# Performance work log

Measured on AMD Instinct MI355X. Metric: run time of the kernel, lower is better.

The kernel has to match this reference:

```python
import jax, jax.numpy as jnp
import numpy as np

BZ, DC, NR = 65536, 512, 1024
MARGIN = 1.0
MASK_VAL = 1000.0

def _l2_normalize(x, eps=1e-12):
    # F.normalize: x / max(||x||_2, eps) along last dim
    n = jnp.sqrt(jnp.sum(x * x, axis=-1, keepdims=True))
    return x / jnp.maximum(n, eps)

def setup_inputs() -> dict:
    key = jax.random.key(0)
    k1, k2, k3 = jax.random.split(key, 3)
    wo = jax.random.normal(k1, (BZ, DC), dtype=jnp.float32)
    rel_weight = jax.random.normal(k2, (NR, DC), dtype=jnp.float32)
    in_y = jax.random.randint(k3, (BZ,), 0, NR, dtype=jnp.int64)
    return {"wo": wo, "rel_weight": rel_weight, "in_y": in_y}

def reference(wo, rel_weight, in_y):
    wo_n = _l2_normalize(wo)                       # [bz, dc]
    rw_n = _l2_normalize(rel_weight)               # [nr, dc]
    # ||a-b|| for unit vectors: sqrt(2 - 2 a.b); avoids [bz,nr,dc] intermediate
    sim = jnp.einsum('bd,nd->bn', wo_n, rw_n)      # [bz, nr]
    all_distance = jnp.sqrt(jnp.maximum(2.0 - 2.0 * sim, 0.0))
    b = jnp.arange(wo.shape[0])
    masked = all_distance.at[b, in_y].add(MASK_VAL)  # mask out the true class
    neg_idx = jnp.argmin(masked, axis=1)           # nearest wrong relation
    # gather instead of one-hot matmul; dist to gathered row equals row of all_distance
    pos_distance = all_distance[b, in_y]
    neg_distance = all_distance[b, neg_idx]
    loss = jnp.mean(pos_distance + jnp.clip(MARGIN - neg_distance, 0.0, 9999.0))
    return loss
```

## Files before the change

### kernel.cpp

```cpp
#include <hip/hip_runtime.h>
#include <stdint.h>

#define BZc 65536
#define DCc 512
#define NRc 1024
#define BM 64
#define NCHUNK 128
#define BCH 4096

typedef float f32x4 __attribute__((ext_vector_type(4)));
typedef const unsigned int __attribute__((address_space(1)))* gas1_t;
typedef unsigned int __attribute__((address_space(3)))* las3_t;

__global__ void __launch_bounds__(64) ndl_prep(const float* __restrict__ rw,
                                               unsigned char* __restrict__ rwn,
                                               float* __restrict__ out) {
    if (blockIdx.x == 0 && threadIdx.x == 0) out[0] = 0.0f;
    const int t = threadIdx.x;
    const int row = blockIdx.x * 8 + (t >> 3);
    const int l8 = t & 7;
    const float4* src = (const float4*)(rw + (size_t)row * DCc) + l8 * 16;
    float4 v[16];
    float ss = 0.0f;
#pragma unroll
    for (int i = 0; i < 16; ++i) {
        v[i] = src[i];
        ss += v[i].x*v[i].x + v[i].y*v[i].y + v[i].z*v[i].z + v[i].w*v[i].w;
    }
    ss += __shfl_xor(ss, 1);
    ss += __shfl_xor(ss, 2);
    ss += __shfl_xor(ss, 4);
    const float inv = rsqrtf(fmaxf(ss, 1e-24f));
    const int swz = ((row >> 2) & 3) << 3;
    char* rowp = (char*)rwn + (size_t)row * DCc;
#pragma unroll
    for (int g = 0; g < 8; ++g) {
        int lo = __builtin_amdgcn_cvt_pk_fp8_f32(v[2*g].x*inv,   v[2*g].y*inv,   0,  false);
        lo     = __builtin_amdgcn_cvt_pk_fp8_f32(v[2*g].z*inv,   v[2*g].w*inv,   lo, true);
        int hi = __builtin_amdgcn_cvt_pk_fp8_f32(v[2*g+1].x*inv, v[2*g+1].y*inv, 0,  false);
        hi     = __builtin_amdgcn_cvt_pk_fp8_f32(v[2*g+1].z*inv, v[2*g+1].w*inv, hi, true);
        int2 pk; pk.x = lo; pk.y = hi;
        *(int2*)(rowp + ((l8 * 64 + g * 8) ^ swz)) = pk;
    }
}

__global__ void __launch_bounds__(256, 3) ndl_main(const float* __restrict__ wo,
                                                   const unsigned char* __restrict__ rwn,
                                                   const long long* __restrict__ iy,
                                                   float* __restrict__ out) {
    __shared__ char As[BM * DCc];
    __shared__ char Bs[4 * BCH];
    __shared__ float invn[BM];
    __shared__ float mxs[BM];
    __shared__ float sys[BM];
    __shared__ float redsum[4];

    const int t = threadIdx.x;
    const int wid = t >> 6;
    const int lane = t & 63;
    const int lm = lane & 15;
    const int lk = lane >> 4;
    const int wm = wid >> 1;
    const int wn = wid & 1;
    const int rbase = blockIdx.x * BM;

    int yrow[2][4];
#pragma unroll
    for (int mt = 0; mt < 2; ++mt)
#pragma unroll
        for (int r = 0; r < 4; ++r)
            yrow[mt][r] = (int)iy[rbase + wm*32 + mt*16 + lk*4 + r];

    {
        const int r = t >> 2;
        const int q = t & 3;
        const float* src = wo + (size_t)(rbase + r) * DCc + q * 128;
        const int swz = (r & 15) << 3;
        char* rowp = As + r * DCc;
        float ss = 0.0f;
#pragma unroll
        for (int g = 0; g < 16; ++g) {
            float4 v0 = *(const float4*)(src + g * 8);
            float4 v1 = *(const float4*)(src + g * 8 + 4);
            ss += v0.x*v0.x + v0.y*v0.y + v0.z*v0.z + v0.w*v0.w
                + v1.x*v1.x + v1.y*v1.y + v1.z*v1.z + v1.w*v1.w;
            int lo = __builtin_amdgcn_cvt_pk_fp8_f32(v0.x, v0.y, 0,  false);
            lo     = __builtin_amdgcn_cvt_pk_fp8_f32(v0.z, v0.w, lo, true);
            int hi = __builtin_amdgcn_cvt_pk_fp8_f32(v1.x, v1.y, 0,  false);
            hi     = __builtin_amdgcn_cvt_pk_fp8_f32(v1.z, v1.w, hi, true);
            int2 pk; pk.x = lo; pk.y = hi;
            *(int2*)(rowp + ((q * 128 + g * 8) ^ swz)) = pk;
        }
        ss += __shfl_xor(ss, 1);
        ss += __shfl_xor(ss, 2);
        if (q == 0) invn[r] = rsqrtf(fmaxf(ss, 1e-24f));
    }
    __syncthreads();

    const int r0 = wm*32 + lm;
    const int r1 = wm*32 + 16 + lm;
    const int arow0 = r0 * DCc, aswz0 = (r0 & 15) << 3;
    const int arow1 = r1 * DCc, aswz1 = (r1 & 15) << 3;
    int boff[4];
#pragma unroll
    for (int nt = 0; nt < 4; ++nt) {
        const int n = wn*64 + nt*16 + lm;
        boff[nt] = n * 32 + ((lk * 8) ^ (((n >> 2) & 3) << 3));
    }
    const unsigned char* bsrc = rwn + (size_t)((wid*32 + (lane >> 1)) * DCc + (lane & 1) * 16);
    char* bdst = Bs + wid * 1024;

#define ISSUE_B(C) do {                                                          \
        const int c_ = (C) & (NCHUNK - 1);                                       \
        __builtin_amdgcn_global_load_lds(                                        \
            (gas1_t)(bsrc + ((c_ >> 4) << 16) + ((c_ & 15) << 5)),               \
            (las3_t)(bdst + (c_ & 3) * BCH), 16, 0, 0);                          \
    } while (0)

    ISSUE_B(0); ISSUE_B(1); ISSUE_B(2);

    f32x4 acc[2][4];
    float mx[2][4], sy[2][4];
#pragma unroll
    for (int mt = 0; mt < 2; ++mt)
#pragma unroll
        for (int nt = 0; nt < 4; ++nt) { f32x4 z = {0.f,0.f,0.f,0.f}; acc[mt][nt] = z; }
#pragma unroll
    for (int mt = 0; mt < 2; ++mt)
#pragma unroll
        for (int r = 0; r < 4; ++r) { mx[mt][r] = -1e30f; sy[mt][r] = -1e30f; }

    for (int c = 0; c < NCHUNK; ++c) {
        asm volatile("s_waitcnt vmcnt(2) lgkmcnt(0)" ::: "memory");
        __builtin_amdgcn_s_barrier();
        __builtin_amdgcn_sched_barrier(0);
        ISSUE_B(c + 3);

        const int kt = c & 15;
        const char* bb = Bs + (c & 3) * BCH;
        const int ka = kt * 32 + lk * 8;
        unsigned long long a0 = *(const unsigned long long*)(As + arow0 + (ka ^ aswz0));
        unsigned long long a1 = *(const unsigned long long*)(As + arow1 + (ka ^ aswz1));
        unsigned long long b0 = *(const unsigned long long*)(bb + boff[0]);
        unsigned long long b1 = *(const unsigned long long*)(bb + boff[1]);
        unsigned long long b2 = *(const unsigned long long*)(bb + boff[2]);
        unsigned long long b3 = *(const unsigned long long*)(bb + boff[3]);
        acc[0][0] = __builtin_amdgcn_mfma_f32_16x16x32_fp8_fp8(a0, b0, acc[0][0], 0, 0, 0);
        acc[0][1] = __builtin_amdgcn_mfma_f32_16x16x32_fp8_fp8(a0, b1, acc[0][1], 0, 0, 0);
        acc[0][2] = __builtin_amdgcn_mfma_f32_16x16x32_fp8_fp8(a0, b2, acc[0][2], 0, 0, 0);
        acc[0][3] = __builtin_amdgcn_mfma_f32_16x16x32_fp8_fp8(a0, b3, acc[0][3], 0, 0, 0);
        acc[1][0] = __builtin_amdgcn_mfma_f32_16x16x32_fp8_fp8(a1, b0, acc[1][0], 0, 0, 0);
        acc[1][1] = __builtin_amdgcn_mfma_f32_16x16x32_fp8_fp8(a1, b1, acc[1][1], 0, 0, 0);
        acc[1][2] = __builtin_amdgcn_mfma_f32_16x16x32_fp8_fp8(a1, b2, acc[1][2], 0, 0, 0);
        acc[1][3] = __builtin_amdgcn_mfma_f32_16x16x32_fp8_fp8(a1, b3, acc[1][3], 0, 0, 0);

        if (kt == 15) {
            const int nb = c >> 4;
#pragma unroll
            for (int mt = 0; mt < 2; ++mt)
#pragma unroll
                for (int nt = 0; nt < 4; ++nt) {
                    const int nglb = nb*128 + wn*64 + nt*16 + lm;
#pragma unroll
                    for (int r = 0; r < 4; ++r) {
                        float s = acc[mt][nt][r];
                        if (nglb == yrow[mt][r]) { sy[mt][r] = s; s = -1e30f; }
                        mx[mt][r] = fmaxf(mx[mt][r], s);
                    }
                    f32x4 z = {0.f,0.f,0.f,0.f};
                    acc[mt][nt] = z;
                }
        }
    }
    asm volatile("s_waitcnt vmcnt(0)" ::: "memory");

#pragma unroll
    for (int d = 1; d <= 8; d <<= 1)
#pragma unroll
        for (int mt = 0; mt < 2; ++mt)
#pragma unroll
            for (int r = 0; r < 4; ++r) {
                mx[mt][r] = fmaxf(mx[mt][r], __shfl_xor(mx[mt][r], d));
                sy[mt][r] = fmaxf(sy[mt][r], __shfl_xor(sy[mt][r], d));
            }
    if (wn == 0 && lm == 0) {
#pragma unroll
        for (int mt = 0; mt < 2; ++mt)
#pragma unroll
            for (int r = 0; r < 4; ++r) {
                const int row = wm*32 + mt*16 + lk*4 + r;
                mxs[row] = mx[mt][r];
                sys[row] = sy[mt][r];
            }
    }
    __syncthreads();
    float csum = 0.0f;
    if (wn == 1 && lm == 0) {
#pragma unroll
        for (int mt = 0; mt < 2; ++mt)
#pragma unroll
            for (int r = 0; r < 4; ++r) {
                const int row = wm*32 + mt*16 + lk*4 + r;
                const float inva = invn[row];
                const float ms  = fmaxf(mx[mt][r], mxs[row]) * inva;
                const float syv = fmaxf(sy[mt][r], sys[row]) * inva;
                const float pos = sqrtf(fmaxf(2.0f - 2.0f * syv, 0.0f));
                const float neg = sqrtf(fmaxf(2.0f - 2.0f * ms, 0.0f));
                csum += pos + fminf(fmaxf(1.0f - neg, 0.0f), 9999.0f);
            }
    }
#pragma unroll
    for (int d = 1; d <= 32; d <<= 1) csum += __shfl_xor(csum, d);
    if (lane == 0) redsum[wid] = csum;
    __syncthreads();
    if (t == 0)
        atomicAdd(out, (redsum[0] + redsum[1] + redsum[2] + redsum[3]) * (1.0f / (float)BZc));
}

extern "C" void kernel_launch(void* const* d_in, const int* in_sizes, int n_in,
                              void* d_out, int out_size, void* d_ws, size_t ws_size,
                              hipStream_t stream) {
    const float* wo = (const float*)d_in[0];
    const float* rw = (const float*)d_in[1];
    const long long* iy = (const long long*)d_in[2];
    float* out = (float*)d_out;
    unsigned char* rwn = (unsigned char*)d_ws;

    ndl_prep<<<NRc / 8, 64, 0, stream>>>(rw, rwn, out);
    ndl_main<<<BZc / BM, 256, 0, stream>>>(wo, rwn, iy, out);
}
```

Measured before the change: 290.1 us.

## Load fp8 relation tiles straight to registers with 32x32 MFMA, drop LDS B pipeline

The prep kernel now writes the normalized fp8 relation matrix in a pre-swizzled layout that matches the 32x32x16 MFMA operand order. Each warp loads its B fragments directly from global/L2 into registers, double-buffered, so the shared-memory B staging ring and its per-chunk barriers go away. The A tile swizzle changes to fit the new MFMA shape, and each warp now owns 32 relation columns against all 64 rows. Launch bounds ask for 4 blocks per CU, the wo loads are nontemporal, and the final reduction goes through shared memory. The risks are more repeated L2 traffic for B and higher register pressure.

```diff
diff --git a/kernel.cpp b/kernel.cpp
--- a/kernel.cpp
+++ b/kernel.cpp
@@ -5,21 +5,21 @@
 #define DCc 512
 #define NRc 1024
 #define BM 64
-#define NCHUNK 128
-#define BCH 4096
 
-typedef float f32x4 __attribute__((ext_vector_type(4)));
-typedef const unsigned int __attribute__((address_space(1)))* gas1_t;
-typedef unsigned int __attribute__((address_space(3)))* las3_t;
+typedef float f32x16 __attribute__((ext_vector_type(16)));
+typedef float f32x4v __attribute__((ext_vector_type(4)));
+typedef unsigned long long u64;
+
+#define ZERO16 {0.f,0.f,0.f,0.f, 0.f,0.f,0.f,0.f, 0.f,0.f,0.f,0.f, 0.f,0.f,0.f,0.f}
 
 __global__ void __launch_bounds__(64) ndl_prep(const float* __restrict__ rw,
                                                unsigned char* __restrict__ rwn,
                                                float* __restrict__ out) {
     if (blockIdx.x == 0 && threadIdx.x == 0) out[0] = 0.0f;
     const int t = threadIdx.x;
-    const int row = blockIdx.x * 8 + (t >> 3);
+    const int n = blockIdx.x * 8 + (t >> 3);
     const int l8 = t & 7;
-    const float4* src = (const float4*)(rw + (size_t)row * DCc) + l8 * 16;
+    const float4* src = (const float4*)(rw + (size_t)n * DCc) + l8 * 16;
     float4 v[16];
     float ss = 0.0f;
 #pragma unroll
@@ -31,65 +31,59 @@
     ss += __shfl_xor(ss, 2);
     ss += __shfl_xor(ss, 4);
     const float inv = rsqrtf(fmaxf(ss, 1e-24f));
-    const int swz = ((row >> 2) & 3) << 3;
-    char* rowp = (char*)rwn + (size_t)row * DCc;
+    unsigned char* base = rwn + ((size_t)(n >> 5) << 14) + (n & 31) * 8;
 #pragma unroll
-    for (int g = 0; g < 8; ++g) {
-        int lo = __builtin_amdgcn_cvt_pk_fp8_f32(v[2*g].x*inv,   v[2*g].y*inv,   0,  false);
-        lo     = __builtin_amdgcn_cvt_pk_fp8_f32(v[2*g].z*inv,   v[2*g].w*inv,   lo, true);
-        int hi = __builtin_amdgcn_cvt_pk_fp8_f32(v[2*g+1].x*inv, v[2*g+1].y*inv, 0,  false);
-        hi     = __builtin_amdgcn_cvt_pk_fp8_f32(v[2*g+1].z*inv, v[2*g+1].w*inv, hi, true);
-        int2 pk; pk.x = lo; pk.y = hi;
-        *(int2*)(rowp + ((l8 * 64 + g * 8) ^ swz)) = pk;
+    for (int p = 0; p < 8; ++p) {
+        float4 v0 = v[2*p], v1 = v[2*p+1];
+        int lo = __builtin_amdgcn_cvt_pk_fp8_f32(v0.x*inv, v0.y*inv, 0,  false);
+        lo     = __builtin_amdgcn_cvt_pk_fp8_f32(v0.z*inv, v0.w*inv, lo, true);
+        int hi8 = __builtin_amdgcn_cvt_pk_fp8_f32(v1.x*inv, v1.y*inv, 0,  false);
+        hi8     = __builtin_amdgcn_cvt_pk_fp8_f32(v1.z*inv, v1.w*inv, hi8, true);
+        int2 pk; pk.x = lo; pk.y = hi8;
+        const int kt = l8*4 + (p >> 1);
+        const int kh = p & 1;
+        *(int2*)(base + kt*512 + kh*256) = pk;
     }
 }
 
-__global__ void __launch_bounds__(256, 3) ndl_main(const float* __restrict__ wo,
+__global__ void __launch_bounds__(256, 4) ndl_main(const float* __restrict__ wo,
                                                    const unsigned char* __restrict__ rwn,
                                                    const long long* __restrict__ iy,
                                                    float* __restrict__ out) {
     __shared__ char As[BM * DCc];
-    __shared__ char Bs[4 * BCH];
     __shared__ float invn[BM];
-    __shared__ float mxs[BM];
-    __shared__ float sys[BM];
-    __shared__ float redsum[4];
+    __shared__ float mxw[4][BM];
+    __shared__ float syw[4][BM];
 
     const int t = threadIdx.x;
     const int wid = t >> 6;
     const int lane = t & 63;
-    const int lm = lane & 15;
-    const int lk = lane >> 4;
-    const int wm = wid >> 1;
-    const int wn = wid & 1;
+    const int l32 = lane & 31;
+    const int hi = lane >> 5;
     const int rbase = blockIdx.x * BM;
 
-    int yrow[2][4];
-#pragma unroll
-    for (int mt = 0; mt < 2; ++mt)
-#pragma unroll
-        for (int r = 0; r < 4; ++r)
-            yrow[mt][r] = (int)iy[rbase + wm*32 + mt*16 + lk*4 + r];
+    int ymnb0 = (int)iy[rbase + l32]      - wid*32 - hi*4;
+    int ymnb1 = (int)iy[rbase + 32 + l32] - wid*32 - hi*4;
 
     {
         const int r = t >> 2;
         const int q = t & 3;
         const float* src = wo + (size_t)(rbase + r) * DCc + q * 128;
-        const int swz = (r & 15) << 3;
+        const int swz = (r & 31) << 3;
         char* rowp = As + r * DCc;
         float ss = 0.0f;
 #pragma unroll
         for (int g = 0; g < 16; ++g) {
-            float4 v0 = *(const float4*)(src + g * 8);
-            float4 v1 = *(const float4*)(src + g * 8 + 4);
+            f32x4v v0 = __builtin_nontemporal_load((const f32x4v*)(src + g*8));
+            f32x4v v1 = __builtin_nontemporal_load((const f32x4v*)(src + g*8 + 4));
             ss += v0.x*v0.x + v0.y*v0.y + v0.z*v0.z + v0.w*v0.w
                 + v1.x*v1.x + v1.y*v1.y + v1.z*v1.z + v1.w*v1.w;
             int lo = __builtin_amdgcn_cvt_pk_fp8_f32(v0.x, v0.y, 0,  false);
             lo     = __builtin_amdgcn_cvt_pk_fp8_f32(v0.z, v0.w, lo, true);
-            int hi = __builtin_amdgcn_cvt_pk_fp8_f32(v1.x, v1.y, 0,  false);
-            hi     = __builtin_amdgcn_cvt_pk_fp8_f32(v1.z, v1.w, hi, true);
-            int2 pk; pk.x = lo; pk.y = hi;
-            *(int2*)(rowp + ((q * 128 + g * 8) ^ swz)) = pk;
+            int hi8 = __builtin_amdgcn_cvt_pk_fp8_f32(v1.x, v1.y, 0,  false);
+            hi8     = __builtin_amdgcn_cvt_pk_fp8_f32(v1.z, v1.w, hi8, true);
+            int2 pk; pk.x = lo; pk.y = hi8;
+            *(int2*)(rowp + ((q*128 + g*8) ^ swz)) = pk;
         }
         ss += __shfl_xor(ss, 1);
         ss += __shfl_xor(ss, 2);
@@ -97,124 +91,83 @@
     }
     __syncthreads();
 
-    const int r0 = wm*32 + lm;
-    const int r1 = wm*32 + 16 + lm;
-    const int arow0 = r0 * DCc, aswz0 = (r0 & 15) << 3;
-    const int arow1 = r1 * DCc, aswz1 = (r1 & 15) << 3;
-    int boff[4];
+    const int aswz = l32 << 3;
+    const char* arow0 = As + l32 * DCc;
+    const char* arow1 = As + (32 + l32) * DCc;
+    const char* bbase = (const char*)rwn + ((size_t)wid << 14) + lane * 8;
+
+    f32x16 acc0 = ZERO16, acc1 = ZERO16;
+    float mx0 = -1e30f, mx1 = -1e30f, sy0 = -1e30f, sy1 = -1e30f;
+
+    auto LOADB = [&](u64* buf, int gi) {
+        const char* gp = bbase + (size_t)(gi >> 2) * 65536 + (gi & 3) * 4096;
 #pragma unroll
-    for (int nt = 0; nt < 4; ++nt) {
-        const int n = wn*64 + nt*16 + lm;
-        boff[nt] = n * 32 + ((lk * 8) ^ (((n >> 2) & 3) << 3));
+        for (int j = 0; j < 8; ++j) buf[j] = *(const u64*)(gp + j * 512);
+    };
+    auto CONSUME = [&](const u64* buf, int gi) {
+        const int ktb = (gi & 3) * 8;
+#pragma unroll
+        for (int j = 0; j < 8; ++j) {
+            const int ko = (ktb + j) * 16 + hi * 8;
+            u64 a0 = *(const u64*)(arow0 + (ko ^ aswz));
+            u64 a1 = *(const u64*)(arow1 + (ko ^ aswz));
+            acc0 = __builtin_amdgcn_mfma_f32_32x32x16_fp8_fp8(buf[j], a0, acc0, 0, 0, 0);
+            acc1 = __builtin_amdgcn_mfma_f32_32x32x16_fp8_fp8(buf[j], a1, acc1, 0, 0, 0);
+        }
+    };
+    auto EPILOGUE = [&]() {
+#pragma unroll
+        for (int reg = 0; reg < 16; ++reg) {
+            const int C = (reg & 3) + 8 * (reg >> 2);
+            float s0 = acc0[reg], s1 = acc1[reg];
+            const bool m0 = (C == ymnb0);
+            const bool m1 = (C == ymnb1);
+            sy0 = m0 ? s0 : sy0;
+            sy1 = m1 ? s1 : sy1;
+            mx0 = fmaxf(mx0, m0 ? -1e30f : s0);
+            mx1 = fmaxf(mx1, m1 ? -1e30f : s1);
+        }
+        f32x16 z = ZERO16;
+        acc0 = z; acc1 = z;
+        ymnb0 -= 128; ymnb1 -= 128;
+    };
+
+    u64 bufA[8], bufB[8];
+    LOADB(bufA, 0);
+#pragma unroll 2
+    for (int io = 0; io < 16; ++io) {
+        const int g0 = 2 * io, g1 = 2 * io + 1;
+        LOADB(bufB, g1);
+        CONSUME(bufA, g0);
+        if (g1 + 1 < 32) LOADB(bufA, g1 + 1);
+        CONSUME(bufB, g1);
+        if ((g1 & 3) == 3) EPILOGUE();
     }
-    const unsigned char* bsrc = rwn + (size_t)((wid*32 + (lane >> 1)) * DCc + (lane & 1) * 16);
-    char* bdst = Bs + wid * 1024;
 
-#define ISSUE_B(C) do {                                                          \
-        const int c_ = (C) & (NCHUNK - 1);                                       \
-        __builtin_amdgcn_global_load_lds(                                        \
-            (gas1_t)(bsrc + ((c_ >> 4) << 16) + ((c_ & 15) << 5)),               \
-            (las3_t)(bdst + (c_ & 3) * BCH), 16, 0, 0);                          \
-    } while (0)
-
-    ISSUE_B(0); ISSUE_B(1); ISSUE_B(2);
-
-    f32x4 acc[2][4];
-    float mx[2][4], sy[2][4];
-#pragma unroll
-    for (int mt = 0; mt < 2; ++mt)
-#pragma unroll
-        for (int nt = 0; nt < 4; ++nt) { f32x4 z = {0.f,0.f,0.f,0.f}; acc[mt][nt] = z; }
-#pragma unroll
-    for (int mt = 0; mt < 2; ++mt)
-#pragma unroll
-        for (int r = 0; r < 4; ++r) { mx[mt][r] = -1e30f; sy[mt][r] = -1e30f; }
-
-    for (int c = 0; c < NCHUNK; ++c) {
-        asm volatile("s_waitcnt vmcnt(2) lgkmcnt(0)" ::: "memory");
-        __builtin_amdgcn_s_barrier();
-        __builtin_amdgcn_sched_barrier(0);
-        ISSUE_B(c + 3);
-
-        const int kt = c & 15;
-        const char* bb = Bs + (c & 3) * BCH;
-        const int ka = kt * 32 + lk * 8;
-        unsigned long long a0 = *(const unsigned long long*)(As + arow0 + (ka ^ aswz0));
-        unsigned long long a1 = *(const unsigned long long*)(As + arow1 + (ka ^ aswz1));
-        unsigned long long b0 = *(const unsigned long long*)(bb + boff[0]);
-        unsigned long long b1 = *(const unsigned long long*)(bb + boff[1]);
-        unsigned long long b2 = *(const unsigned long long*)(bb + boff[2]);
-        unsigned long long b3 = *(const unsigned long long*)(bb + boff[3]);
-        acc[0][0] = __builtin_amdgcn_mfma_f32_16x16x32_fp8_fp8(a0, b0, acc[0][0], 0, 0, 0);
-        acc[0][1] = __builtin_amdgcn_mfma_f32_16x16x32_fp8_fp8(a0, b1, acc[0][1], 0, 0, 0);
-        acc[0][2] = __builtin_amdgcn_mfma_f32_16x16x32_fp8_fp8(a0, b2, acc[0][2], 0, 0, 0);
-        acc[0][3] = __builtin_amdgcn_mfma_f32_16x16x32_fp8_fp8(a0, b3, acc[0][3], 0, 0, 0);
-        acc[1][0] = __builtin_amdgcn_mfma_f32_16x16x32_fp8_fp8(a1, b0, acc[1][0], 0, 0, 0);
-        acc[1][1] = __builtin_amdgcn_mfma_f32_16x16x32_fp8_fp8(a1, b1, acc[1][1], 0, 0, 0);
-        acc[1][2] = __builtin_amdgcn_mfma_f32_16x16x32_fp8_fp8(a1, b2, acc[1][2], 0, 0, 0);
-        acc[1][3] = __builtin_amdgcn_mfma_f32_16x16x32_fp8_fp8(a1, b3, acc[1][3], 0, 0, 0);
-
-        if (kt == 15) {
-            const int nb = c >> 4;
-#pragma unroll
-            for (int mt = 0; mt < 2; ++mt)
-#pragma unroll
-                for (int nt = 0; nt < 4; ++nt) {
-                    const int nglb = nb*128 + wn*64 + nt*16 + lm;
-#pragma unroll
-                    for (int r = 0; r < 4; ++r) {
-                        float s = acc[mt][nt][r];
-                        if (nglb == yrow[mt][r]) { sy[mt][r] = s; s = -1e30f; }
-                        mx[mt][r] = fmaxf(mx[mt][r], s);
-                    }
-                    f32x4 z = {0.f,0.f,0.f,0.f};
-                    acc[mt][nt] = z;
-                }
-        }
-    }
-    asm volatile("s_waitcnt vmcnt(0)" ::: "memory");
-
-#pragma unroll
-    for (int d = 1; d <= 8; d <<= 1)
-#pragma unroll
-        for (int mt = 0; mt < 2; ++mt)
-#pragma unroll
-            for (int r = 0; r < 4; ++r) {
-                mx[mt][r] = fmaxf(mx[mt][r], __shfl_xor(mx[mt][r], d));
-                sy[mt][r] = fmaxf(sy[mt][r], __shfl_xor(sy[mt][r], d));
-            }
-    if (wn == 0 && lm == 0) {
-#pragma unroll
-        for (int mt = 0; mt < 2; ++mt)
-#pragma unroll
-            for (int r = 0; r < 4; ++r) {
-                const int row = wm*32 + mt*16 + lk*4 + r;
-                mxs[row] = mx[mt][r];
-                sys[row] = sy[mt][r];
-            }
+    mx0 = fmaxf(mx0, __shfl_xor(mx0, 32));
+    mx1 = fmaxf(mx1, __shfl_xor(mx1, 32));
+    sy0 = fmaxf(sy0, __shfl_xor(sy0, 32));
+    sy1 = fmaxf(sy1, __shfl_xor(sy1, 32));
+    if (hi == 0) {
+        mxw[wid][l32]      = mx0;
+        mxw[wid][32 + l32] = mx1;
+        syw[wid][l32]      = sy0;
+        syw[wid][32 + l32] = sy1;
     }
     __syncthreads();
-    float csum = 0.0f;
-    if (wn == 1 && lm == 0) {
+
+    if (wid == 0) {
+        float ms = fmaxf(fmaxf(mxw[0][lane], mxw[1][lane]), fmaxf(mxw[2][lane], mxw[3][lane]));
+        float sv = fmaxf(fmaxf(syw[0][lane], syw[1][lane]), fmaxf(syw[2][lane], syw[3][lane]));
+        const float ia = invn[lane];
+        ms *= ia; sv *= ia;
+        const float pos = sqrtf(fmaxf(2.0f - 2.0f * sv, 0.0f));
+        const float neg = sqrtf(fmaxf(2.0f - 2.0f * ms, 0.0f));
+        float c = pos + fminf(fmaxf(1.0f - neg, 0.0f), 9999.0f);
 #pragma unroll
-        for (int mt = 0; mt < 2; ++mt)
-#pragma unroll
-            for (int r = 0; r < 4; ++r) {
-                const int row = wm*32 + mt*16 + lk*4 + r;
-                const float inva = invn[row];
-                const float ms  = fmaxf(mx[mt][r], mxs[row]) * inva;
-                const float syv = fmaxf(sy[mt][r], sys[row]) * inva;
-                const float pos = sqrtf(fmaxf(2.0f - 2.0f * syv, 0.0f));
-                const float neg = sqrtf(fmaxf(2.0f - 2.0f * ms, 0.0f));
-                csum += pos + fminf(fmaxf(1.0f - neg, 0.0f), 9999.0f);
-            }
+        for (int d = 1; d <= 32; d <<= 1) c += __shfl_xor(c, d);
+        if (lane == 0) atomicAdd(out, c * (1.0f / (float)BZc));
     }
-#pragma unroll
-    for (int d = 1; d <= 32; d <<= 1) csum += __shfl_xor(csum, d);
-    if (lane == 0) redsum[wid] = csum;
-    __syncthreads();
-    if (t == 0)
-        atomicAdd(out, (redsum[0] + redsum[1] + redsum[2] + redsum[3]) * (1.0f / (float)BZc));
 }
 
 extern "C" void kernel_launch(void* const* d_in, const int* in_sizes, int n_in,
```

After: 380.7 us. 31.2% more time.
